# Optimization experiments

Measured on AMD Instinct MI355X. Metric: run time of the kernel, lower is better.

Reference implementation:

```python
import jax, jax.numpy as jnp
import numpy as np

DIM = 128
HEADS = 8
HD = DIM // HEADS          # 16
KS = 8                     # neighborhood kernel size
STRIDE = 2                 # GNA query-group stride
DIL = 2                    # dilation


def axis_indices(L, k, s, d):
    """Per-axis neighborhood indices [L, k] for dilated, strided, edge-clamped NA.

    Queries are grouped in blocks of `s`; every query in a block shares the
    window of the block's center query (GNA 'stride'). Dilation partitions the
    axis into `d` sub-grids; the window lives on the center query's sub-grid
    and is clamped so it never leaves the axis (natten-style sliding window).
    """
    idx = np.zeros((L, k), dtype=np.int32)
    for i in range(L):
        ic = min((i // s) * s + (s - 1) // 2, L - 1)   # group-center query
        r = ic % d                                      # sub-grid (residue)
        Lsub = (L - r + d - 1) // d                     # sub-grid length
        ii = ic // d                                    # index within sub-grid
        start = min(max(ii - (k - 1) // 2, 0), max(Lsub - k, 0))
        for j in range(k):
            idx[i, j] = r + d * min(start + j, Lsub - 1)
    return idx


def setup_inputs() -> dict:
    key = jax.random.key(0)
    ks = jax.random.split(key, 5)
    x = jax.random.normal(ks[0], (1, DIM, 96, 96), jnp.float32)
    # depthwise-grouped qkv conv: Conv2d(dim, 3*dim, 3, 1, 1, groups=dim)
    qkv_w = jax.random.normal(ks[1], (3 * DIM, 1, 3, 3), jnp.float32) * 0.1
    qkv_b = jax.random.normal(ks[2], (3 * DIM,), jnp.float32) * 0.02
    # 1x1 projection: Conv2d(dim, dim, 1)
    proj_w = jax.random.normal(ks[3], (DIM, DIM, 1, 1), jnp.float32) * (DIM ** -0.5)
    proj_b = jax.random.normal(ks[4], (DIM,), jnp.float32) * 0.02
    return {"x": x, "qkv_w": qkv_w, "qkv_b": qkv_b, "proj_w": proj_w, "proj_b": proj_b}


def reference(x, qkv_w, qkv_b, proj_w, proj_b):
    B, C, H, W = x.shape
    # grouped (groups=C) 3x3 conv producing q,k,v
    qkv = jax.lax.conv_general_dilated(
        x, qkv_w, window_strides=(1, 1), padding=[(1, 1), (1, 1)],
        dimension_numbers=("NCHW", "OIHW", "NCHW"), feature_group_count=C)
    qkv = qkv + qkv_b[None, :, None, None]
    qkv = qkv.reshape(B, 3, C, H, W)

    def to_heads(t):  # b c h w -> b h w nh hd
        return t.reshape(B, HEADS, HD, H, W).transpose(0, 3, 4, 1, 2)

    q = to_heads(qkv[:, 0])
    k = to_heads(qkv[:, 1])
    v = to_heads(qkv[:, 2])

    scale = HD ** -0.5
    ri = jnp.asarray(axis_indices(H, KS, STRIDE, DIL))  # [H, KS]
    ci = jnp.asarray(axis_indices(W, KS, STRIDE, DIL))  # [W, KS]
    R = ri[:, :, None, None]       # [H, KS, 1, 1]
    Cc = ci[None, None, :, :]      # [1, 1, W, KS]
    k_win = k[:, R, Cc]            # [B, H, KS, W, KS, nh, hd]
    v_win = v[:, R, Cc]

    logits = jnp.einsum("bijnd,bipjqnd->bijnpq", q * scale, k_win)
    attn = jax.nn.softmax(logits.reshape(B, H, W, HEADS, KS * KS), axis=-1)
    attn = attn.reshape(B, H, W, HEADS, KS, KS)
    out = jnp.einsum("bijnpq,bipjqnd->bijnd", attn, v_win)

    out = out.transpose(0, 3, 4, 1, 2).reshape(B, C, H, W)  # b h w nh hd -> b c h w
    out = jnp.einsum("bchw,oc->bohw", out, proj_w[:, :, 0, 0]) + proj_b[None, :, None, None]
    return out
```

## Files before the change

kernel.cpp:

```cpp
#include <hip/hip_runtime.h>
#include <hip/hip_bf16.h>

#define HH   96
#define WW   96
#define NPIX 9216
#define CH   128
#define NH   8
#define HD   16
#define KS   8

#define NPOS    120
#define KVPITCH 40
#define PMPITCH 392

__device__ __forceinline__ unsigned short f2bf(float f) {
    __hip_bfloat16 b = __float2bfloat16(f);
    union { __hip_bfloat16 b; unsigned short u; } cv; cv.b = b; return cv.u;
}
__device__ __forceinline__ void u4_to_f8(uint4 u, float* f) {
    f[0] = __uint_as_float(u.x << 16); f[1] = __uint_as_float(u.x & 0xffff0000u);
    f[2] = __uint_as_float(u.y << 16); f[3] = __uint_as_float(u.y & 0xffff0000u);
    f[4] = __uint_as_float(u.z << 16); f[5] = __uint_as_float(u.z & 0xffff0000u);
    f[6] = __uint_as_float(u.w << 16); f[7] = __uint_as_float(u.w & 0xffff0000u);
}

__global__ __launch_bounds__(256) void conv_pm_kernel(
    const float* __restrict__ x,
    const float* __restrict__ w,
    const float* __restrict__ bias,
    unsigned short* __restrict__ qkv_pm)
{
    __shared__ unsigned short ldst[24 * PMPITCH];

    const int row = blockIdx.x >> 2;
    const int q   = blockIdx.x & 3;
    const int j0q = q * 24;
    const int tid = threadIdx.x;
    const int g   = tid >> 1;
    const int sh  = tid & 1;
    const int j0  = j0q + sh * 12;

    const float* xg = x + g * NPIX;

    float xr[3][14];
    #pragma unroll
    for (int dr = 0; dr < 3; ++dr) {
        const int r = row + dr - 1;
        if (r >= 0 && r < HH) {
            #pragma unroll
            for (int m = 0; m < 14; ++m) {
                const int j = j0 + m - 1;
                xr[dr][m] = (j >= 0 && j < WW) ? xg[r * WW + j] : 0.f;
            }
        } else {
            #pragma unroll
            for (int m = 0; m < 14; ++m) xr[dr][m] = 0.f;
        }
    }

    #pragma unroll
    for (int dt = 0; dt < 3; ++dt) {
        const int o = 3 * g + dt;
        float w9[9];
        #pragma unroll
        for (int k = 0; k < 9; ++k) w9[k] = w[o * 9 + k];
        const float b = bias[o];

        #pragma unroll
        for (int px = 0; px < 12; ++px) {
            float acc = b;
            #pragma unroll
            for (int kh = 0; kh < 3; ++kh)
                #pragma unroll
                for (int kw = 0; kw < 3; ++kw)
                    acc += xr[kh][px + kw] * w9[kh * 3 + kw];
            ldst[(sh * 12 + px) * PMPITCH + o] = f2bf(acc);
        }
    }

    __syncthreads();

    #pragma unroll
    for (int it = 0; it < 5; ++it) {
        const int idx = it * 256 + tid;
        if (idx < 1152) {
            const int px = idx / 48;
            const int c8 = idx - px * 48;
            const int o  = c8 * 8;
            const uint4 v = *(const uint4*)&ldst[px * PMPITCH + o];
            const int t = o >> 7, c = o & 127;
            *(uint4*)(qkv_pm + ((size_t)t * NPIX + row * WW + j0q + px) * CH + c) = v;
        }
    }
}

__global__ __launch_bounds__(256) void attn_kernel(
    const unsigned short* __restrict__ qkv_pm,
    float* __restrict__ a_t)
{
    __shared__ unsigned short kv[2][NPOS * KVPITCH];

    const int tid = threadIdx.x;
    const int seg = blockIdx.x;
    const int hp  = blockIdx.y;
    const int i   = seg / 6;
    const int j0  = (seg - i * 6) * 16;
    const int rs     = 2 * min(max(i / 2 - 3, 0), 40);
    const int cs_min = 2 * min(max(j0 / 2 - 3, 0), 40);

    #pragma unroll
    for (int it = 0; it < 4; ++it) {
        const int idx = it * 256 + tid;
        if (idx < 960) {
            const int kvsel = idx / 480;
            const int rem   = idx - kvsel * 480;
            const int pos   = rem >> 2;
            const int sub   = rem & 3;
            const int p     = pos / 15;
            const int cc    = pos - p * 15;
            const int pixg  = (rs + 2 * p) * WW + cs_min + 2 * cc;
            *(uint4*)&kv[kvsel][pos * KVPITCH + sub * 8] =
                *(const uint4*)(qkv_pm + ((size_t)(1 + kvsel) * NPIX + pixg) * CH
                                + hp * 32 + sub * 8);
        }
    }

    const int lane  = tid & 63;
    const int wave  = tid >> 6;
    const int r     = lane >> 3;
    const int hh    = (lane >> 2) & 1;
    const int px    = wave * 4 + (lane & 3);
    const int h     = hp * 2 + hh;
    const int pix   = seg * 16 + px;
    const int j     = j0 + px;
    const int ci0   = (2 * min(max(j / 2 - 3, 0), 40) - cs_min) >> 1;

    float qr[HD];
    {
        const unsigned short* qp = qkv_pm + (size_t)pix * CH + h * HD;
        u4_to_f8(*(const uint4*)qp, qr);
        u4_to_f8(*(const uint4*)(qp + 8), qr + 8);
        #pragma unroll
        for (int d = 0; d < HD; ++d) qr[d] *= 0.25f;
    }

    __syncthreads();

    const int posr = r * 15 + ci0;
    float lg[KS];
    float m = -1e30f;
    #pragma unroll
    for (int q = 0; q < KS; ++q) {
        const unsigned short* kp = &kv[0][(posr + q) * KVPITCH + hh * HD];
        float kf[HD];
        u4_to_f8(*(const uint4*)kp, kf);
        u4_to_f8(*(const uint4*)(kp + 8), kf + 8);
        float acc = 0.f;
        #pragma unroll
        for (int d = 0; d < HD; ++d) acc += qr[d] * kf[d];
        lg[q] = acc;
        m = fmaxf(m, acc);
    }

    float s = 0.f;
    #pragma unroll
    for (int q = 0; q < KS; ++q) { lg[q] = __expf(lg[q] - m); s += lg[q]; }

    float o[HD];
    #pragma unroll
    for (int d = 0; d < HD; ++d) o[d] = 0.f;
    #pragma unroll
    for (int q = 0; q < KS; ++q) {
        const unsigned short* vp = &kv[1][(posr + q) * KVPITCH + hh * HD];
        float vf[HD];
        u4_to_f8(*(const uint4*)vp, vf);
        u4_to_f8(*(const uint4*)(vp + 8), vf + 8);
        const float wgt = lg[q];
        #pragma unroll
        for (int d = 0; d < HD; ++d) o[d] += wgt * vf[d];
    }

    #pragma unroll
    for (int mask = 8; mask <= 32; mask <<= 1) {
        const float m2 = __shfl_xor(m, mask);
        const float s2 = __shfl_xor(s, mask);
        const float mn = fmaxf(m, m2);
        const float ea = __expf(m - mn);
        const float eb = __expf(m2 - mn);
        s = s * ea + s2 * eb;
        #pragma unroll
        for (int d = 0; d < HD; ++d) {
            const float o2 = __shfl_xor(o[d], mask);
            o[d] = o[d] * ea + o2 * eb;
        }
        m = mn;
    }
    const float inv = 1.f / s;

    a_t[(size_t)(h * HD + 2 * r)     * NPIX + pix] = o[2 * r]     * inv;
    a_t[(size_t)(h * HD + 2 * r + 1) * NPIX + pix] = o[2 * r + 1] * inv;
}

__global__ __launch_bounds__(256) void proj_kernel(
    const float* __restrict__ a_t,
    const float* __restrict__ pw,
    const float* __restrict__ pb,
    float* __restrict__ out)
{
    const int idx = blockIdx.x * 256 + threadIdx.x;
    const int op  = __builtin_amdgcn_readfirstlane(idx / 2304);
    const int pq  = idx - op * 2304;
    const int px0 = pq * 4;
    const int o0  = op * 2;

    float acc0[4], acc1[4];
    #pragma unroll
    for (int e = 0; e < 4; ++e) { acc0[e] = pb[o0]; acc1[e] = pb[o0 + 1]; }

    for (int c = 0; c < CH; ++c) {
        const float4 a  = *(const float4*)(a_t + (size_t)c * NPIX + px0);
        const float  w0 = pw[(o0)     * CH + c];
        const float  w1 = pw[(o0 + 1) * CH + c];
        acc0[0] += a.x * w0; acc0[1] += a.y * w0; acc0[2] += a.z * w0; acc0[3] += a.w * w0;
        acc1[0] += a.x * w1; acc1[1] += a.y * w1; acc1[2] += a.z * w1; acc1[3] += a.w * w1;
    }

    *(float4*)(out + (size_t)(o0)     * NPIX + px0) = make_float4(acc0[0], acc0[1], acc0[2], acc0[3]);
    *(float4*)(out + (size_t)(o0 + 1) * NPIX + px0) = make_float4(acc1[0], acc1[1], acc1[2], acc1[3]);
}

extern "C" void kernel_launch(void* const* d_in, const int* in_sizes, int n_in,
                              void* d_out, int out_size, void* d_ws, size_t ws_size,
                              hipStream_t stream)
{
    const float* x      = (const float*)d_in[0];
    const float* qkv_w  = (const float*)d_in[1];
    const float* qkv_b  = (const float*)d_in[2];
    const float* proj_w = (const float*)d_in[3];
    const float* proj_b = (const float*)d_in[4];
    float* out = (float*)d_out;

    unsigned short* qkv_pm = (unsigned short*)d_ws;
    float*          a_t    = (float*)(qkv_pm + 3 * NPIX * CH);

    conv_pm_kernel<<<384, 256, 0, stream>>>(x, qkv_w, qkv_b, qkv_pm);
    attn_kernel   <<<dim3(576, 4), 256, 0, stream>>>(qkv_pm, a_t);
    proj_kernel   <<<576, 256, 0, stream>>>(a_t, proj_w, proj_b, out);
}
```

Baseline: 105.6 us.

## Compute and store K/V only at even-row/even-column pixels used by attention

With the dilation and stride pattern, attention only reads K and V at even rows and even columns. The conv kernel now computes K/V only for those pixels and writes them to a compact 48x48 buffer, while Q is still written at full resolution. This cuts conv arithmetic and global traffic for K/V and makes the attention kernel's K/V loads denser. In exchange, work is uneven across conv blocks, since odd rows skip the K/V part.

```diff
diff --git a/kernel.cpp b/kernel.cpp
--- a/kernel.cpp
+++ b/kernel.cpp
@@ -9,9 +9,11 @@
 #define HD   16
 #define KS   8
 
+#define NEPIX   2304
 #define NPOS    120
 #define KVPITCH 40
-#define PMPITCH 392
+#define QTPITCH 136
+#define KVTPITCH 264
 
 __device__ __forceinline__ unsigned short f2bf(float f) {
     __hip_bfloat16 b = __float2bfloat16(f);
@@ -24,21 +26,24 @@
     f[6] = __uint_as_float(u.w << 16); f[7] = __uint_as_float(u.w & 0xffff0000u);
 }
 
-__global__ __launch_bounds__(256) void conv_pm_kernel(
+__global__ __launch_bounds__(256) void conv_kernel(
     const float* __restrict__ x,
     const float* __restrict__ w,
     const float* __restrict__ bias,
-    unsigned short* __restrict__ qkv_pm)
-{
-    __shared__ unsigned short ldst[24 * PMPITCH];
+    unsigned short* __restrict__ q_pm,
+    unsigned short* __restrict__ kv_pm)
+{
+    __shared__ unsigned short qt [24 * QTPITCH];
+    __shared__ unsigned short kvt[12 * KVTPITCH];
 
     const int row = blockIdx.x >> 2;
-    const int q   = blockIdx.x & 3;
-    const int j0q = q * 24;
+    const int qtr = blockIdx.x & 3;
+    const int j0q = qtr * 24;
     const int tid = threadIdx.x;
     const int g   = tid >> 1;
     const int sh  = tid & 1;
     const int j0  = j0q + sh * 12;
+    const bool kvrow = (row & 1) == 0;
 
     const float* xg = x + g * NPIX;
 
@@ -61,41 +66,66 @@
     #pragma unroll
     for (int dt = 0; dt < 3; ++dt) {
         const int o = 3 * g + dt;
+        const int t = o >> 7;
+        const int c = o & 127;
         float w9[9];
         #pragma unroll
         for (int k = 0; k < 9; ++k) w9[k] = w[o * 9 + k];
         const float b = bias[o];
 
-        #pragma unroll
-        for (int px = 0; px < 12; ++px) {
-            float acc = b;
-            #pragma unroll
-            for (int kh = 0; kh < 3; ++kh)
+        if (t == 0) {
+            #pragma unroll
+            for (int px = 0; px < 12; ++px) {
+                float acc = b;
                 #pragma unroll
-                for (int kw = 0; kw < 3; ++kw)
-                    acc += xr[kh][px + kw] * w9[kh * 3 + kw];
-            ldst[(sh * 12 + px) * PMPITCH + o] = f2bf(acc);
+                for (int kh = 0; kh < 3; ++kh)
+                    #pragma unroll
+                    for (int kw = 0; kw < 3; ++kw)
+                        acc += xr[kh][px + kw] * w9[kh * 3 + kw];
+                qt[(sh * 12 + px) * QTPITCH + c] = f2bf(acc);
+            }
+        } else if (kvrow) {
+            #pragma unroll
+            for (int pe = 0; pe < 6; ++pe) {
+                const int px = pe * 2;
+                float acc = b;
+                #pragma unroll
+                for (int kh = 0; kh < 3; ++kh)
+                    #pragma unroll
+                    for (int kw = 0; kw < 3; ++kw)
+                        acc += xr[kh][px + kw] * w9[kh * 3 + kw];
+                kvt[(sh * 6 + pe) * KVTPITCH + (t - 1) * CH + c] = f2bf(acc);
+            }
         }
     }
 
     __syncthreads();
 
-    #pragma unroll
-    for (int it = 0; it < 5; ++it) {
+    const int ntask = kvrow ? 768 : 384;
+    #pragma unroll
+    for (int it = 0; it < 3; ++it) {
         const int idx = it * 256 + tid;
-        if (idx < 1152) {
-            const int px = idx / 48;
-            const int c8 = idx - px * 48;
-            const int o  = c8 * 8;
-            const uint4 v = *(const uint4*)&ldst[px * PMPITCH + o];
-            const int t = o >> 7, c = o & 127;
-            *(uint4*)(qkv_pm + ((size_t)t * NPIX + row * WW + j0q + px) * CH + c) = v;
+        if (idx < 384) {
+            const int px  = idx >> 4;
+            const int c8  = (idx & 15) * 8;
+            const uint4 v = *(const uint4*)&qt[px * QTPITCH + c8];
+            *(uint4*)(q_pm + ((size_t)(row * WW) + j0q + px) * CH + c8) = v;
+        } else if (idx < ntask) {
+            const int k2  = idx - 384;
+            const int epx = k2 >> 5;
+            const int c32 = (k2 & 31) * 8;
+            const int t1  = c32 >> 7;
+            const int c   = c32 & 127;
+            const uint4 v = *(const uint4*)&kvt[epx * KVTPITCH + c32];
+            *(uint4*)(kv_pm + ((size_t)t1 * NEPIX + (row >> 1) * 48
+                               + (j0q >> 1) + epx) * CH + c) = v;
         }
     }
 }
 
 __global__ __launch_bounds__(256) void attn_kernel(
-    const unsigned short* __restrict__ qkv_pm,
+    const unsigned short* __restrict__ q_pm,
+    const unsigned short* __restrict__ kv_pm,
     float* __restrict__ a_t)
 {
     __shared__ unsigned short kv[2][NPOS * KVPITCH];
@@ -107,6 +137,8 @@
     const int j0  = (seg - i * 6) * 16;
     const int rs     = 2 * min(max(i / 2 - 3, 0), 40);
     const int cs_min = 2 * min(max(j0 / 2 - 3, 0), 40);
+    const int er0 = rs >> 1;
+    const int ec0 = cs_min >> 1;
 
     #pragma unroll
     for (int it = 0; it < 4; ++it) {
@@ -118,9 +150,10 @@
             const int sub   = rem & 3;
             const int p     = pos / 15;
             const int cc    = pos - p * 15;
-            const int pixg  = (rs + 2 * p) * WW + cs_min + 2 * cc;
+            const int ec    = min(ec0 + cc, 47);
+            const int ep    = (er0 + p) * 48 + ec;
             *(uint4*)&kv[kvsel][pos * KVPITCH + sub * 8] =
-                *(const uint4*)(qkv_pm + ((size_t)(1 + kvsel) * NPIX + pixg) * CH
+                *(const uint4*)(kv_pm + ((size_t)kvsel * NEPIX + ep) * CH
                                 + hp * 32 + sub * 8);
         }
     }
@@ -137,7 +170,7 @@
 
     float qr[HD];
     {
-        const unsigned short* qp = qkv_pm + (size_t)pix * CH + h * HD;
+        const unsigned short* qp = q_pm + (size_t)pix * CH + h * HD;
         u4_to_f8(*(const uint4*)qp, qr);
         u4_to_f8(*(const uint4*)(qp + 8), qr + 8);
         #pragma unroll
@@ -240,10 +273,11 @@
     const float* proj_b = (const float*)d_in[4];
     float* out = (float*)d_out;
 
-    unsigned short* qkv_pm = (unsigned short*)d_ws;
-    float*          a_t    = (float*)(qkv_pm + 3 * NPIX * CH);
-
-    conv_pm_kernel<<<384, 256, 0, stream>>>(x, qkv_w, qkv_b, qkv_pm);
-    attn_kernel   <<<dim3(576, 4), 256, 0, stream>>>(qkv_pm, a_t);
-    proj_kernel   <<<576, 256, 0, stream>>>(a_t, proj_w, proj_b, out);
-}
+    unsigned short* q_pm  = (unsigned short*)d_ws;
+    unsigned short* kv_pm = q_pm + (size_t)NPIX * CH;
+    float*          a_t   = (float*)(kv_pm + (size_t)2 * NEPIX * CH);
+
+    conv_kernel<<<384, 256, 0, stream>>>(x, qkv_w, qkv_b, q_pm, kv_pm);
+    attn_kernel<<<dim3(576, 4), 256, 0, stream>>>(q_pm, kv_pm, a_t);
+    proj_kernel<<<576, 256, 0, stream>>>(a_t, proj_w, proj_b, out);
+}
```

New measurement: 103.5 us. -2.0%, faster.
